# Kernel tuning notes

Measured on AMD Instinct MI355X. Metric: run time of the kernel, lower is better.

Reference implementation:

```python
import jax, jax.numpy as jnp
import numpy as np

N, D, HID, G, E2 = 2048, 256, 128, 8, 16384


def _mlp(h, w1, b1, g, be, w2, b2):
    # Linear -> ReLU -> BatchNorm1d (training mode, biased batch var) -> Linear
    h = jax.nn.relu(h @ w1 + b1)
    mu = h.mean(axis=0)
    var = ((h - mu) ** 2).mean(axis=0)
    h = (h - mu) / jnp.sqrt(var + 1e-5) * g + be
    return h @ w2 + b2


def setup_inputs() -> dict:
    key = jax.random.key(0)
    ks = jax.random.split(key, 12)
    x = jax.random.normal(ks[0], (N, D), jnp.float32)
    src = jax.random.randint(ks[1], (E2,), 0, N)
    dst = jax.random.randint(ks[2], (E2,), 0, N)
    src = jnp.where(src == dst, (src + 1) % N, src)  # no self loops
    edge_index = jnp.stack([jnp.concatenate([src, dst]),
                            jnp.concatenate([dst, src])])  # symmetric
    batch = jnp.sort(jax.random.randint(ks[3], (N,), 0, G))
    def lin(k, i, o):
        return 0.1 * jax.random.normal(k, (i, o), jnp.float32)
    out = dict(x=x, edge_index=edge_index, batch=batch)
    dims = [(1, HID, HID), (HID, HID, HID), (HID, HID, 1)]
    names = [("w11", "b11", "g1", "be1", "w12", "b12"),
             ("w21", "b21", "g2", "be2", "w22", "b22"),
             ("w31", "b31", "g3", "be3", "w32", "b32")]
    k = 4
    for (i, h, o), n in zip(dims, names):
        out[n[0]] = lin(ks[k], i, h)
        out[n[1]] = jnp.zeros((h,), jnp.float32)
        out[n[2]] = jnp.ones((h,), jnp.float32)
        out[n[3]] = jnp.zeros((h,), jnp.float32)
        out[n[4]] = lin(ks[k + 1], h, o)
        out[n[5]] = jnp.zeros((o,), jnp.float32)
        k += 2
    return out


def reference(x, edge_index, batch,
              w11, b11, g1, be1, w12, b12,
              w21, b21, g2, be2, w22, b22,
              w31, b31, g3, be3, w32, b32):
    n = x.shape[0]
    # dense adjacency from edge_index; L = D - A (unnormalized graph Laplacian)
    A = jnp.zeros((n, n), x.dtype).at[edge_index[0], edge_index[1]].set(1.0)
    deg = A.sum(axis=1)
    # entropy term: V = x*(Lx) - x*(Ax) + A(x*x), Lx = deg*x - Ax
    Ax = A @ x
    V = x * (deg[:, None] * x - Ax) - x * Ax + A @ (x * x)
    V = jnp.linalg.norm(V, axis=1)  # [n]
    # per-graph softmax over the batch segments
    mx = jax.ops.segment_max(V, batch, num_segments=G)
    ex = jnp.exp(V - mx[batch])
    P = ex / jax.ops.segment_sum(ex, batch, num_segments=G)[batch]
    P = jnp.where(P == 0.0, 1.0, P)
    ent = -P * jnp.log(P)  # [n]

    # GINConv (eps=0): mlp(x + sum_{j in N(i)} x_j) = mlp(x + A @ x)
    def gin(h, w1, b1, g, be, w2, b2):
        return _mlp(h + A @ h, w1, b1, g, be, w2, b2)

    h = gin(ent[:, None], w11, b11, g1, be1, w12, b12)
    h = gin(h, w21, b21, g2, be2, w22, b22)
    h = gin(h, w31, b31, g3, be3, w32, b32)
    p = jax.nn.sigmoid(h[:, 0])  # [n] node probabilities

    gamma = ent.sum()
    loss = gamma - jnp.vdot(ent, p) + jnp.vdot(p, A @ p)

    # greedy conditional expectation (sequential MIS-style selection)
    order = jnp.argsort(-p)

    def step(carry, idx):
        dummy, sel, rej = carry
        nb = A[idx] > 0.0  # neighbor mask [n]
        deg0 = ~jnp.any(nb)
        sel = sel.at[idx].set(sel[idx] | deg0)  # isolated node -> selected
        eligible = (~rej[idx]) & (~sel[idx])
        s = jnp.where(nb, 0.0, dummy).at[idx].set(1.0)
        li = gamma - jnp.vdot(ent, s) + jnp.vdot(s, A @ s)
        accept = eligible & (li <= loss)
        sel = sel.at[idx].set(sel[idx] | accept)
        rej = rej | (nb & accept)
        dummy = jnp.where(accept, s, dummy)
        return (dummy, sel, rej), None

    init = (p, jnp.zeros(n, dtype=bool), jnp.zeros(n, dtype=bool))
    (dummy, sel, rej), _ = jax.lax.scan(step, init, order)

    # graph reconstruction (masked instead of compacted, for static shapes)
    mask = sel.astype(x.dtype)
    x_pooled = x * mask[:, None]
    A2 = A @ A
    A3 = A2 @ A
    eye = jnp.eye(n, dtype=x.dtype)
    adj_pooled = (1.0 - eye) * jnp.clip(A2 + A3, 0.0, 1.0) * (mask[:, None] * mask[None, :])
    batch_pooled = jnp.where(sel, batch, -1)
    return x_pooled, adj_pooled, sel, batch_pooled, loss
```

## Files before the change

### kernel.cpp

```cpp
#include <hip/hip_runtime.h>
#include <math.h>

#define NN 2048
#define DIMF 256
#define HIDN 128
#define NG 8
#define NEDGES 32768
#define W32 32
#define TRI_CAP 131072
#define TRI_LDS 4864

typedef unsigned long long u64;
typedef unsigned char u8;
typedef unsigned short u16;

__global__ void k_init(u64* __restrict__ rowbits, int* __restrict__ segstart) {
  int i = blockIdx.x * blockDim.x + threadIdx.x;
  for (int k = i; k < NN * W32; k += gridDim.x * blockDim.x) rowbits[k] = 0ull;
  if (i <= NG) segstart[i] = NN;
}

__global__ void k_edges(const int* __restrict__ ei, u64* __restrict__ rowbits) {
  int e = blockIdx.x * blockDim.x + threadIdx.x;
  if (e >= NEDGES) return;
  int u = ei[e], v = ei[NEDGES + e];
  atomicOr(&rowbits[((size_t)u << 5) + (v >> 6)], 1ull << (v & 63));
}

__global__ void k_deg(const u64* __restrict__ rowbits, int* __restrict__ deg,
                      const int* __restrict__ batch, int* __restrict__ segstart) {
  int i = blockIdx.x * blockDim.x + threadIdx.x;
  if (i >= NN) return;
  int c = 0;
  for (int w = 0; w < W32; ++w) c += __popcll(rowbits[(i << 5) + w]);
  deg[i] = c;
  if (i == 0 || batch[i] != batch[i - 1]) segstart[batch[i]] = i;
}

__global__ void k_scan2048(const int* __restrict__ in, int* __restrict__ out) {
  __shared__ int part[256];
  int t = threadIdx.x;
  int v[8]; int s = 0;
  for (int k = 0; k < 8; ++k) { v[k] = in[t * 8 + k]; s += v[k]; }
  part[t] = s;
  __syncthreads();
  for (int off = 1; off < 256; off <<= 1) {
    int y = (t >= off) ? part[t - off] : 0;
    __syncthreads();
    part[t] += y;
    __syncthreads();
  }
  int run = part[t] - s;
  for (int k = 0; k < 8; ++k) { out[t * 8 + k] = run; run += v[k]; }
  if (t == 255) out[NN] = part[255];
}

__global__ void k_extract(const u64* __restrict__ rowbits, const int* __restrict__ rp,
                          int* __restrict__ col, int* __restrict__ cnt) {
  int i = blockIdx.x * blockDim.x + threadIdx.x;
  if (i >= NN) return;
  const u64* ri = rowbits + ((size_t)i << 5);
  int o = rp[i];
  for (int w = 0; w < W32; ++w) {
    u64 b = ri[w];
    while (b) { col[o++] = (w << 6) + __builtin_ctzll(b); b &= b - 1; }
  }
  int c = 0;
  for (int e = rp[i]; e < o; ++e) {
    const u64* ra = rowbits + ((size_t)col[e] << 5);
    for (int w = 0; w < W32; ++w) c += __popcll(ra[w] & ri[w]);
  }
  cnt[i] = c;
}

__global__ void k_trifill(const u64* __restrict__ rowbits, const int* __restrict__ rp,
                          const int* __restrict__ col, const int* __restrict__ tp,
                          int2* __restrict__ tri) {
  int i = blockIdx.x * blockDim.x + threadIdx.x;
  if (i >= NN) return;
  const u64* ri = rowbits + ((size_t)i << 5);
  int o = tp[i];
  for (int e = rp[i]; e < rp[i + 1]; ++e) {
    int a = col[e];
    const u64* ra = rowbits + ((size_t)a << 5);
    for (int w = 0; w < W32; ++w) {
      u64 b = ra[w] & ri[w];
      while (b) {
        int j = (w << 6) + __builtin_ctzll(b);
        if (o < TRI_CAP) tri[o] = make_int2(a, j);
        ++o;
        b &= b - 1;
      }
    }
  }
}

__global__ void k_V(const float* __restrict__ x, const int* __restrict__ rp,
                    const int* __restrict__ col, float* __restrict__ V) {
  int i = blockIdx.x; int t = threadIdx.x;
  float xi = x[i * DIMF + t];
  float s1 = 0.f, s2 = 0.f;
  int r0 = rp[i], r1 = rp[i + 1];
  for (int e = r0; e < r1; ++e) {
    float xj = x[col[e] * DIMF + t];
    s1 += xj; s2 += xj * xj;
  }
  float dg = (float)(r1 - r0);
  float val = dg * xi * xi - 2.f * xi * s1 + s2;
  __shared__ double red[DIMF];
  red[t] = (double)val * (double)val;
  __syncthreads();
  for (int off = DIMF / 2; off > 0; off >>= 1) { if (t < off) red[t] += red[t + off]; __syncthreads(); }
  if (t == 0) V[i] = (float)sqrt(red[0]);
}

__global__ void k_soft(const float* __restrict__ V, const int* __restrict__ segstart,
                       float* __restrict__ ent, double* __restrict__ seggamma) {
  int g = blockIdx.x; int t = threadIdx.x;
  int s = segstart[g];
  int e = NN;
  for (int gg = g + 1; gg <= NG; ++gg) { int v = segstart[gg]; if (v < e) e = v; }
  if (s >= e) { if (t == 0) seggamma[g] = 0.0; return; }
  __shared__ float fm[256];
  __shared__ double dd[256];
  float m = -3.0e38f;
  for (int i = s + t; i < e; i += 256) m = fmaxf(m, V[i]);
  fm[t] = m; __syncthreads();
  for (int off = 128; off > 0; off >>= 1) { if (t < off) fm[t] = fmaxf(fm[t], fm[t + off]); __syncthreads(); }
  float mx = fm[0];
  __syncthreads();
  double sum = 0.0;
  for (int i = s + t; i < e; i += 256) sum += exp((double)V[i] - (double)mx);
  dd[t] = sum; __syncthreads();
  for (int off = 128; off > 0; off >>= 1) { if (t < off) dd[t] += dd[t + off]; __syncthreads(); }
  double tot = dd[0];
  __syncthreads();
  double gs = 0.0;
  for (int i = s + t; i < e; i += 256) {
    double P = exp((double)V[i] - (double)mx) / tot;
    float ev = (P > 0.0) ? (float)(-P * log(P)) : 0.f;
    ent[i] = ev;
    gs += (double)ev;
  }
  dd[t] = gs; __syncthreads();
  for (int off = 128; off > 0; off >>= 1) { if (t < off) dd[t] += dd[t + off]; __syncthreads(); }
  if (t == 0) seggamma[g] = dd[0];
}

__global__ void k_agg1(const float* __restrict__ ent, const int* __restrict__ rp,
                       const int* __restrict__ col, float* __restrict__ agg) {
  int i = blockIdx.x * blockDim.x + threadIdx.x;
  if (i >= NN) return;
  float a = ent[i];
  for (int e = rp[i]; e < rp[i + 1]; ++e) a += ent[col[e]];
  agg[i] = a;
}

template<int FROMAGG>
__global__ void k_bn(const float* __restrict__ src, const float* __restrict__ w1,
                     const float* __restrict__ b1, const float* __restrict__ g,
                     const float* __restrict__ be, float* __restrict__ scale,
                     float* __restrict__ shift) {
  int k = blockIdx.x; int tid = threadIdx.x;
  __shared__ double red[256];
  float wk = 0.f, bk = 0.f;
  if (FROMAGG) { wk = w1[k]; bk = b1[k]; }
  double s = 0.0;
  for (int i = tid; i < NN; i += 256) {
    float v;
    if (FROMAGG) { v = src[i] * wk + bk; v = v > 0.f ? v : 0.f; }
    else v = src[i * HIDN + k];
    s += (double)v;
  }
  red[tid] = s; __syncthreads();
  for (int off = 128; off > 0; off >>= 1) { if (tid < off) red[tid] += red[tid + off]; __syncthreads(); }
  double mu = red[0] / NN;
  __syncthreads();
  double vv = 0.0;
  for (int i = tid; i < NN; i += 256) {
    float v;
    if (FROMAGG) { v = src[i] * wk + bk; v = v > 0.f ? v : 0.f; }
    else v = src[i * HIDN + k];
    double dv = (double)v - mu; vv += dv * dv;
  }
  red[tid] = vv; __syncthreads();
  for (int off = 128; off > 0; off >>= 1) { if (tid < off) red[tid] += red[tid + off]; __syncthreads(); }
  if (tid == 0) {
    float var = (float)(red[0] / NN);
    float sc = g[k] / sqrtf(var + 1e-5f);
    scale[k] = sc;
    shift[k] = be[k] - (float)mu * sc;
  }
}

template<int PRE, int RELU>
__global__ void k_mm(const float* __restrict__ in, const float* __restrict__ Wm,
                     const float* __restrict__ bias, const float* __restrict__ scale,
                     const float* __restrict__ shift, const float* __restrict__ lw,
                     const float* __restrict__ lb, float* __restrict__ out) {
  __shared__ float ti[8][HIDN];
  int r0 = blockIdx.x * 8; int t = threadIdx.x;
  for (int r = 0; r < 8; ++r) {
    float v;
    if (PRE == 2) {
      v = in[r0 + r] * lw[t] + lb[t];
      v = v > 0.f ? v : 0.f;
      v = v * scale[t] + shift[t];
    } else {
      v = in[(r0 + r) * HIDN + t];
      if (PRE == 1) v = v * scale[t] + shift[t];
    }
    ti[r][t] = v;
  }
  __syncthreads();
  float acc[8];
  #pragma unroll
  for (int r = 0; r < 8; ++r) acc[r] = 0.f;
  for (int k = 0; k < HIDN; ++k) {
    float w = Wm[k * HIDN + t];
    #pragma unroll
    for (int r = 0; r < 8; ++r) acc[r] += ti[r][k] * w;
  }
  for (int r = 0; r < 8; ++r) {
    float v = acc[r] + bias[t];
    if (RELU) v = fmaxf(v, 0.f);
    out[(r0 + r) * HIDN + t] = v;
  }
}

__global__ void k_agg128(const float* __restrict__ h, const int* __restrict__ rp,
                         const int* __restrict__ col, float* __restrict__ agg) {
  int i = blockIdx.x; int t = threadIdx.x;
  float a = h[i * HIDN + t];
  for (int e = rp[i]; e < rp[i + 1]; ++e) a += h[col[e] * HIDN + t];
  agg[i * HIDN + t] = a;
}

__global__ void k_lin3(const float* __restrict__ tn, const float* __restrict__ scale,
                       const float* __restrict__ shift, const float* __restrict__ w32,
                       const float* __restrict__ b32, float* __restrict__ p) {
  int i = blockIdx.x; int t = threadIdx.x;
  float v = (tn[i * HIDN + t] * scale[t] + shift[t]) * w32[t];
  __shared__ float red[HIDN];
  red[t] = v; __syncthreads();
  for (int off = 64; off > 0; off >>= 1) { if (t < off) red[t] += red[t + off]; __syncthreads(); }
  if (t == 0) {
    float h3 = red[0] + b32[0];
    p[i] = 1.f / (1.f + expf(-h3));
  }
}

__global__ void k_q0(const float* __restrict__ p, const float* __restrict__ ent,
                     const int* __restrict__ rp, const int* __restrict__ col,
                     float* __restrict__ q0, float* __restrict__ e0) {
  int i = blockIdx.x * blockDim.x + threadIdx.x;
  if (i >= NN) return;
  float s = 0.f, es = 0.f;
  for (int e = rp[i]; e < rp[i + 1]; ++e) {
    int j = col[e];
    float pj = p[j];
    s += pj; es += ent[j] * pj;
  }
  q0[i] = s; e0[i] = es;
}

__global__ void __launch_bounds__(1024, 1) k_sortloss(
    const float* __restrict__ p, const float* __restrict__ ent,
    const float* __restrict__ q0, const double* __restrict__ seggamma,
    double* __restrict__ scal, int* __restrict__ order) {
  __shared__ u64 s[NN];
  __shared__ double rr[32];
  int t = threadIdx.x;
  double a = 0.0, b = 0.0;
  for (int i = t; i < NN; i += 1024) {
    a += (double)ent[i] * (double)p[i];
    b += (double)p[i] * (double)q0[i];
  }
  for (int off = 32; off; off >>= 1) { a += __shfl_down(a, off); b += __shfl_down(b, off); }
  if ((t & 63) == 0) { rr[(t >> 6) * 2] = a; rr[(t >> 6) * 2 + 1] = b; }
  for (int k = t; k < NN; k += 1024) {
    unsigned bb = __float_as_uint(p[k]);
    unsigned ss = (bb & 0x80000000u) ? ~bb : (bb | 0x80000000u);
    s[k] = ((u64)(~ss) << 32) | (unsigned)k;
  }
  __syncthreads();
  if (t == 0) {
    double A = 0.0, Bb = 0.0, gamma = 0.0;
    for (int i = 0; i < 16; ++i) { A += rr[2 * i]; Bb += rr[2 * i + 1]; }
    for (int g = 0; g < NG; ++g) gamma += seggamma[g];
    scal[0] = gamma; scal[1] = A; scal[2] = Bb; scal[3] = gamma - A + Bb;
  }
  for (int k = 2; k <= NN; k <<= 1) {
    for (int j = k >> 1; j > 0; j >>= 1) {
      for (int i = t; i < NN; i += 1024) {
        int ixj = i ^ j;
        if (ixj > i) {
          bool up = ((i & k) == 0);
          u64 aa = s[i], bb = s[ixj];
          if ((aa > bb) == up) { s[i] = bb; s[ixj] = aa; }
        }
      }
      __syncthreads();
    }
  }
  order[t] = (int)(s[t] & 0xFFFFFFFFull);
  order[t + 1024] = (int)(s[t + 1024] & 0xFFFFFFFFull);
}

#define DPP2(ctrl)                                                                        \
  a += __int_as_float(__builtin_amdgcn_update_dpp(0, __float_as_int(a), ctrl, 0xf, 0xf, true)); \
  b += __int_as_float(__builtin_amdgcn_update_dpp(0, __float_as_int(b), ctrl, 0xf, 0xf, true));

__device__ __forceinline__ void red2(float& a, float& b) {
  DPP2(0x111)
  DPP2(0x112)
  DPP2(0x114)
  DPP2(0x118)
  DPP2(0x142)
  DPP2(0x143)
  a = __int_as_float(__builtin_amdgcn_readlane(__float_as_int(a), 63));
  b = __int_as_float(__builtin_amdgcn_readlane(__float_as_int(b), 63));
}

__global__ void __launch_bounds__(1024, 1) k_greedy(
    const int* __restrict__ rp, const int* __restrict__ col,
    const int* __restrict__ tp, const int2* __restrict__ tri,
    const int* __restrict__ order, const float* __restrict__ p,
    const float* __restrict__ ent, const float* __restrict__ q0,
    const float* __restrict__ e0, const double* __restrict__ scal,
    u8* __restrict__ selb_g) {
  __shared__ float2 dq[NN];
  __shared__ float2 ee[NN];
  __shared__ u16 colL[NEDGES];
  __shared__ u16 ordl[NN];
  __shared__ uint2 rtP[NN + 1];
  __shared__ ushort2 triL[TRI_LDS];
  __shared__ unsigned decidedL[64], selL[64];
  __shared__ unsigned maskL[2];
  __shared__ float4 svA[2][16];
  __shared__ float svQ[2][16];
  int t = threadIdx.x;
  int w = t >> 6, lane = t & 63;

  for (int i = t; i < NN; i += 1024) {
    dq[i] = make_float2(p[i], q0[i]);
    ee[i] = make_float2(ent[i], e0[i]);
    ordl[i] = (u16)order[i];
    int tv0 = tp[i]; if (tv0 > 65535) tv0 = 65535;
    int tv1 = tp[i + 1]; if (tv1 > 65535) tv1 = 65535;
    rtP[i] = make_uint2((unsigned)rp[i] | ((unsigned)tv0 << 16),
                        (unsigned)rp[i + 1] | ((unsigned)tv1 << 16));
  }
  for (int i = t; i < NEDGES; i += 1024) colL[i] = (u16)col[i];
  for (int i = t; i < TRI_LDS; i += 1024) {
    int2 ab = tri[i];
    triL[i] = make_ushort2((u16)(ab.x & 2047), (u16)(ab.y & 2047));
  }
  if (t < 64) { decidedL[t] = 0u; selL[t] = 0u; }
  if (t < 2) maskL[t] = 0u;
  double gamma = scal[0], loss = scal[3];
  double ed = scal[1], dAd = scal[2];
  __syncthreads();
  for (int i = t; i < NN; i += 1024) {
    if (((rtP[i].y & 0xffffu) - (rtP[i].x & 0xffffu)) == 0u) {
      atomicOr(&decidedL[i >> 5], 1u << (i & 31));
      atomicOr(&selL[i >> 5], 1u << (i & 31));
    }
  }
  __syncthreads();

  int pos = 0, rc = 0;
  while (pos < NN) {
    int b = rc & 1; ++rc;
    int step = pos + w;
    if (step < NN) {
      int idx = ordl[step];
      if (!((decidedL[idx >> 5] >> (idx & 31)) & 1u)) {
        uint2 rt = rtP[idx];
        int r0 = rt.x & 0xffff, r1 = rt.y & 0xffff;
        int t0 = rt.x >> 16, t1 = rt.y >> 16;
        float2 dqi = dq[idx];
        float2 eei = ee[idx];
        float s2 = 0.f, st = 0.f;
        for (int e = r0 + lane; e < r1; e += 64) {
          float2 v = dq[colL[e]];
          s2 -= v.y * v.x;
        }
        if (t1 <= TRI_LDS) {
          for (int e = t0 + lane; e < t1; e += 64) {
            ushort2 ab = triL[e];
            st += dq[ab.x].x * dq[ab.y].x;
          }
        } else {
          int g0 = tp[idx], g1 = tp[idx + 1];
          if (g0 > TRI_CAP) g0 = TRI_CAP;
          if (g1 > TRI_CAP) g1 = TRI_CAP;
          for (int e = g0 + lane; e < g1; e += 64) {
            int2 ab = tri[e];
            st += dq[ab.x].x * dq[ab.y].x;
          }
        }
        red2(s2, st);
        float d0 = 1.f - dqi.x;
        float S1 = -eei.y + eei.x * d0;
        float S2 = s2 + dqi.y * d0;
        float sn = -dqi.y;
        double cross = 2.0 * (double)d0 * (double)sn + (double)st;
        double li = gamma - (ed + (double)S1) + (dAd + 2.0 * (double)S2 + cross);
        if (li <= loss && lane == 0) {
          svA[b][w] = make_float4(S1, S2, d0, st);
          svQ[b][w] = dqi.y;
          atomicOr(&maskL[b], 1u << w);
        }
      }
    }
    __syncthreads();
    unsigned mask = maskL[b];
    if (mask == 0u) { pos += 16; continue; }
    int k = __builtin_ctz(mask);
    int idx = ordl[pos + k];
    float4 A = svA[b][k];
    float qi = svQ[b][k];
    uint2 rt = rtP[idx];
    int r0 = rt.x & 0xffff, r1 = rt.y & 0xffff;
    {
      double cross = 2.0 * (double)A.z * (double)(-qi) + (double)A.w;
      ed += (double)A.x;
      dAd += 2.0 * (double)A.y + cross;
    }
    for (int e = r0 + w; e < r1; e += 16) {
      int a = colL[e];
      float da = -dq[a].x;
      if (da != 0.f) {
        float ea = ee[a].x;
        uint2 art = rtP[a];
        int b0 = art.x & 0xffff, b1 = art.y & 0xffff;
        for (int eb = b0 + lane; eb < b1; eb += 64) {
          int bb = colL[eb];
          atomicAdd(&dq[bb].y, da);
          atomicAdd(&ee[bb].y, ea * da);
        }
      }
    }
    {
      float ei = ee[idx].x;
      for (int e = r0 + t; e < r1; e += 1024) {
        int bb = colL[e];
        atomicAdd(&dq[bb].y, A.z);
        atomicAdd(&ee[bb].y, ei * A.z);
      }
    }
    __syncthreads();
    if (t == 0) {
      dq[idx].x = 1.f;
      atomicOr(&decidedL[idx >> 5], 1u << (idx & 31));
      atomicOr(&selL[idx >> 5], 1u << (idx & 31));
      maskL[b] = 0u;
    }
    for (int e = r0 + t; e < r1; e += 1024) {
      int j = colL[e];
      dq[j].x = 0.f;
      atomicOr(&decidedL[j >> 5], 1u << (j & 31));
    }
    __syncthreads();
    pos = pos + k + 1;
  }
  for (int i = t; i < NN; i += 1024)
    selb_g[i] = (u8)((selL[i >> 5] >> (i & 31)) & 1u);
}

__global__ void k_reach(const u64* __restrict__ src, const int* __restrict__ rp,
                        const int* __restrict__ col, u64* __restrict__ dst) {
  int node = blockIdx.x * 2 + (threadIdx.x >> 5);
  int w = threadIdx.x & 31;
  u64 acc = 0;
  for (int e = rp[node]; e < rp[node + 1]; ++e) acc |= src[((size_t)col[e] << 5) + w];
  dst[((size_t)node << 5) + w] = acc;
}

__global__ void k_out(const u64* __restrict__ row2, const u64* __restrict__ row3,
                      const u8* __restrict__ selb, const float* __restrict__ x,
                      const int* __restrict__ batch, const double* __restrict__ scal,
                      float* __restrict__ o_x, float* __restrict__ o_adj,
                      float* __restrict__ o_sel, float* __restrict__ o_bat,
                      float* __restrict__ o_loss) {
  int idx = blockIdx.x * blockDim.x + threadIdx.x;
  {
    int i = idx >> 11, j = idx & 2047;
    int wo = (i << 5) + (j >> 6);
    u64 b = (row2[wo] | row3[wo]) >> (j & 63);
    o_adj[idx] = ((b & 1ull) && i != j && selb[i] && selb[j]) ? 1.f : 0.f;
  }
  if (idx < NN * DIMF) {
    int i = idx >> 8;
    o_x[idx] = selb[i] ? x[idx] : 0.f;
  }
  if (idx < NN) {
    o_sel[idx] = selb[idx] ? 1.f : 0.f;
    o_bat[idx] = selb[idx] ? (float)batch[idx] : -1.f;
  }
  if (idx == 0) o_loss[0] = (float)scal[3];
}

extern "C" void kernel_launch(void* const* d_in, const int* in_sizes, int n_in,
                              void* d_out, int out_size, void* d_ws, size_t ws_size,
                              hipStream_t stream) {
  const float* x    = (const float*)d_in[0];
  const int*   ei   = (const int*)d_in[1];
  const int*   batch= (const int*)d_in[2];
  const float* w11  = (const float*)d_in[3];
  const float* b11  = (const float*)d_in[4];
  const float* g1   = (const float*)d_in[5];
  const float* be1  = (const float*)d_in[6];
  const float* w12  = (const float*)d_in[7];
  const float* b12  = (const float*)d_in[8];
  const float* w21  = (const float*)d_in[9];
  const float* b21  = (const float*)d_in[10];
  const float* g2   = (const float*)d_in[11];
  const float* be2  = (const float*)d_in[12];
  const float* w22  = (const float*)d_in[13];
  const float* b22  = (const float*)d_in[14];
  const float* w31  = (const float*)d_in[15];
  const float* b31  = (const float*)d_in[16];
  const float* g3   = (const float*)d_in[17];
  const float* be3  = (const float*)d_in[18];
  const float* w32  = (const float*)d_in[19];
  const float* b32  = (const float*)d_in[20];

  char* wsb = (char*)d_ws;
  size_t cur = 0;
  auto alloc = [&](size_t bytes) -> void* {
    void* pp = wsb + cur;
    cur += (bytes + 255) & ~(size_t)255;
    return pp;
  };
  u64*    rowbits = (u64*)alloc((size_t)NN * W32 * 8);
  u64*    row2    = (u64*)alloc((size_t)NN * W32 * 8);
  u64*    row3    = (u64*)alloc((size_t)NN * W32 * 8);
  double* seggam  = (double*)alloc(NG * 8);
  double* scal    = (double*)alloc(4 * 8);
  int*    deg     = (int*)alloc(NN * 4);
  int*    rowptr  = (int*)alloc((NN + 1) * 4);
  int*    colx    = (int*)alloc(65536 * 4);
  int*    tricnt  = (int*)alloc(NN * 4);
  int*    triptr  = (int*)alloc((NN + 1) * 4);
  int2*   tri     = (int2*)alloc((size_t)TRI_CAP * 8);
  int*    segst   = (int*)alloc((NG + 1) * 4);
  int*    order   = (int*)alloc(NN * 4);
  float*  ent     = (float*)alloc(NN * 4);
  float*  V       = (float*)alloc(NN * 4);
  float*  p       = (float*)alloc(NN * 4);
  float*  q0      = (float*)alloc(NN * 4);
  float*  e0      = (float*)alloc(NN * 4);
  float*  agg1    = (float*)alloc(NN * 4);
  float*  scale   = (float*)alloc(HIDN * 4);
  float*  shift   = (float*)alloc(HIDN * 4);
  float*  tA      = (float*)alloc((size_t)NN * HIDN * 4);
  float*  tB      = (float*)alloc((size_t)NN * HIDN * 4);
  float*  tC      = (float*)alloc((size_t)NN * HIDN * 4);
  u8*     selb    = (u8*)alloc(NN);

  float* out    = (float*)d_out;
  float* o_x    = out;
  float* o_adj  = out + 524288;
  float* o_sel  = out + 4718592;
  float* o_bat  = out + 4720640;
  float* o_loss = out + 4722688;

  k_init<<<64, 256, 0, stream>>>(rowbits, segst);
  k_edges<<<128, 256, 0, stream>>>(ei, rowbits);
  k_deg<<<8, 256, 0, stream>>>(rowbits, deg, batch, segst);
  k_scan2048<<<1, 256, 0, stream>>>(deg, rowptr);
  k_extract<<<8, 256, 0, stream>>>(rowbits, rowptr, colx, tricnt);
  k_scan2048<<<1, 256, 0, stream>>>(tricnt, triptr);
  k_trifill<<<8, 256, 0, stream>>>(rowbits, rowptr, colx, triptr, tri);
  k_V<<<NN, 256, 0, stream>>>(x, rowptr, colx, V);
  k_soft<<<NG, 256, 0, stream>>>(V, segst, ent, seggam);

  k_agg1<<<8, 256, 0, stream>>>(ent, rowptr, colx, agg1);
  k_bn<1><<<HIDN, 256, 0, stream>>>(agg1, w11, b11, g1, be1, scale, shift);
  k_mm<2, 0><<<NN / 8, HIDN, 0, stream>>>(agg1, w12, b12, scale, shift, w11, b11, tB);
  k_agg128<<<NN, HIDN, 0, stream>>>(tB, rowptr, colx, tC);
  k_mm<0, 1><<<NN / 8, HIDN, 0, stream>>>(tC, w21, b21, scale, shift, (const float*)0, (const float*)0, tA);
  k_bn<0><<<HIDN, 256, 0, stream>>>(tA, (const float*)0, (const float*)0, g2, be2, scale, shift);
  k_mm<1, 0><<<NN / 8, HIDN, 0, stream>>>(tA, w22, b22, scale, shift, (const float*)0, (const float*)0, tB);
  k_agg128<<<NN, HIDN, 0, stream>>>(tB, rowptr, colx, tC);
  k_mm<0, 1><<<NN / 8, HIDN, 0, stream>>>(tC, w31, b31, scale, shift, (const float*)0, (const float*)0, tA);
  k_bn<0><<<HIDN, 256, 0, stream>>>(tA, (const float*)0, (const float*)0, g3, be3, scale, shift);
  k_lin3<<<NN, HIDN, 0, stream>>>(tA, scale, shift, w32, b32, p);

  k_q0<<<8, 256, 0, stream>>>(p, ent, rowptr, colx, q0, e0);
  k_sortloss<<<1, 1024, 0, stream>>>(p, ent, q0, seggam, scal, order);
  k_greedy<<<1, 1024, 0, stream>>>(rowptr, colx, triptr, tri, order, p, ent, q0, e0, scal, selb);

  k_reach<<<NN / 2, 64, 0, stream>>>(rowbits, rowptr, colx, row2);
  k_reach<<<NN / 2, 64, 0, stream>>>(row2, rowptr, colx, row3);
  k_out<<<NN * NN / 256, 256, 0, stream>>>(row2, row3, selb, x, batch, scal,
                                           o_x, o_adj, o_sel, o_bat, o_loss);

  (void)in_sizes; (void)n_in; (void)out_size; (void)ws_size;
}
```

Before: 1.091 ms.

## Compact undecided candidates in greedy loop and fold q0/loss/degree-scan kernels

```diff
diff --git a/kernel.cpp b/kernel.cpp
--- a/kernel.cpp
+++ b/kernel.cpp
@@ -27,14 +27,29 @@
   atomicOr(&rowbits[((size_t)u << 5) + (v >> 6)], 1ull << (v & 63));
 }
 
-__global__ void k_deg(const u64* __restrict__ rowbits, int* __restrict__ deg,
-                      const int* __restrict__ batch, int* __restrict__ segstart) {
-  int i = blockIdx.x * blockDim.x + threadIdx.x;
-  if (i >= NN) return;
-  int c = 0;
-  for (int w = 0; w < W32; ++w) c += __popcll(rowbits[(i << 5) + w]);
-  deg[i] = c;
-  if (i == 0 || batch[i] != batch[i - 1]) segstart[batch[i]] = i;
+__global__ void k_degscan(const u64* __restrict__ rowbits, const int* __restrict__ batch,
+                          int* __restrict__ segstart, int* __restrict__ out) {
+  __shared__ int part[256];
+  int t = threadIdx.x;
+  int v[8]; int s = 0;
+  for (int k = 0; k < 8; ++k) {
+    int node = t * 8 + k;
+    int c = 0;
+    for (int w = 0; w < W32; ++w) c += __popcll(rowbits[((size_t)node << 5) + w]);
+    v[k] = c; s += c;
+    if (node == 0 || batch[node] != batch[node - 1]) segstart[batch[node]] = node;
+  }
+  part[t] = s;
+  __syncthreads();
+  for (int off = 1; off < 256; off <<= 1) {
+    int y = (t >= off) ? part[t - off] : 0;
+    __syncthreads();
+    part[t] += y;
+    __syncthreads();
+  }
+  int run = part[t] - s;
+  for (int k = 0; k < 8; ++k) { out[t * 8 + k] = run; run += v[k]; }
+  if (t == 255) out[NN] = part[255];
 }
 
 __global__ void k_scan2048(const int* __restrict__ in, int* __restrict__ out) {
@@ -250,54 +265,24 @@
   }
 }
 
-__global__ void k_q0(const float* __restrict__ p, const float* __restrict__ ent,
-                     const int* __restrict__ rp, const int* __restrict__ col,
-                     float* __restrict__ q0, float* __restrict__ e0) {
-  int i = blockIdx.x * blockDim.x + threadIdx.x;
-  if (i >= NN) return;
-  float s = 0.f, es = 0.f;
-  for (int e = rp[i]; e < rp[i + 1]; ++e) {
-    int j = col[e];
-    float pj = p[j];
-    s += pj; es += ent[j] * pj;
-  }
-  q0[i] = s; e0[i] = es;
-}
-
-__global__ void __launch_bounds__(1024, 1) k_sortloss(
-    const float* __restrict__ p, const float* __restrict__ ent,
-    const float* __restrict__ q0, const double* __restrict__ seggamma,
-    double* __restrict__ scal, int* __restrict__ order) {
+__global__ void __launch_bounds__(1024, 1) k_sort(const float* __restrict__ p,
+                                                  int* __restrict__ order) {
   __shared__ u64 s[NN];
-  __shared__ double rr[32];
   int t = threadIdx.x;
-  double a = 0.0, b = 0.0;
-  for (int i = t; i < NN; i += 1024) {
-    a += (double)ent[i] * (double)p[i];
-    b += (double)p[i] * (double)q0[i];
-  }
-  for (int off = 32; off; off >>= 1) { a += __shfl_down(a, off); b += __shfl_down(b, off); }
-  if ((t & 63) == 0) { rr[(t >> 6) * 2] = a; rr[(t >> 6) * 2 + 1] = b; }
   for (int k = t; k < NN; k += 1024) {
-    unsigned bb = __float_as_uint(p[k]);
-    unsigned ss = (bb & 0x80000000u) ? ~bb : (bb | 0x80000000u);
+    unsigned b = __float_as_uint(p[k]);
+    unsigned ss = (b & 0x80000000u) ? ~b : (b | 0x80000000u);
     s[k] = ((u64)(~ss) << 32) | (unsigned)k;
   }
   __syncthreads();
-  if (t == 0) {
-    double A = 0.0, Bb = 0.0, gamma = 0.0;
-    for (int i = 0; i < 16; ++i) { A += rr[2 * i]; Bb += rr[2 * i + 1]; }
-    for (int g = 0; g < NG; ++g) gamma += seggamma[g];
-    scal[0] = gamma; scal[1] = A; scal[2] = Bb; scal[3] = gamma - A + Bb;
-  }
   for (int k = 2; k <= NN; k <<= 1) {
     for (int j = k >> 1; j > 0; j >>= 1) {
       for (int i = t; i < NN; i += 1024) {
         int ixj = i ^ j;
         if (ixj > i) {
           bool up = ((i & k) == 0);
-          u64 aa = s[i], bb = s[ixj];
-          if ((aa > bb) == up) { s[i] = bb; s[ixj] = aa; }
+          u64 a = s[i], b = s[ixj];
+          if ((a > b) == up) { s[i] = b; s[ixj] = a; }
         }
       }
       __syncthreads();
@@ -326,9 +311,8 @@
     const int* __restrict__ rp, const int* __restrict__ col,
     const int* __restrict__ tp, const int2* __restrict__ tri,
     const int* __restrict__ order, const float* __restrict__ p,
-    const float* __restrict__ ent, const float* __restrict__ q0,
-    const float* __restrict__ e0, const double* __restrict__ scal,
-    u8* __restrict__ selb_g) {
+    const float* __restrict__ ent, const double* __restrict__ seggam,
+    double* __restrict__ scal, u8* __restrict__ selb_g) {
   __shared__ float2 dq[NN];
   __shared__ float2 ee[NN];
   __shared__ u16 colL[NEDGES];
@@ -339,12 +323,15 @@
   __shared__ unsigned maskL[2];
   __shared__ float4 svA[2][16];
   __shared__ float svQ[2][16];
+  __shared__ int   svP[2][16];
+  __shared__ u64 wbalL[16];
+  __shared__ double rr[36];
   int t = threadIdx.x;
   int w = t >> 6, lane = t & 63;
 
   for (int i = t; i < NN; i += 1024) {
-    dq[i] = make_float2(p[i], q0[i]);
-    ee[i] = make_float2(ent[i], e0[i]);
+    dq[i].x = p[i];
+    ee[i].x = ent[i];
     ordl[i] = (u16)order[i];
     int tv0 = tp[i]; if (tv0 > 65535) tv0 = 65535;
     int tv1 = tp[i + 1]; if (tv1 > 65535) tv1 = 65535;
@@ -358,69 +345,129 @@
   }
   if (t < 64) { decidedL[t] = 0u; selL[t] = 0u; }
   if (t < 2) maskL[t] = 0u;
-  double gamma = scal[0], loss = scal[3];
-  double ed = scal[1], dAd = scal[2];
   __syncthreads();
   for (int i = t; i < NN; i += 1024) {
-    if (((rtP[i].y & 0xffffu) - (rtP[i].x & 0xffffu)) == 0u) {
+    int r0 = rtP[i].x & 0xffff, r1 = rtP[i].y & 0xffff;
+    float qs = 0.f, es = 0.f;
+    for (int e = r0; e < r1; ++e) {
+      int j = colL[e];
+      float pj = dq[j].x;
+      qs += pj; es += ee[j].x * pj;
+    }
+    dq[i].y = qs; ee[i].y = es;
+    if (r0 == r1) {
       atomicOr(&decidedL[i >> 5], 1u << (i & 31));
       atomicOr(&selL[i >> 5], 1u << (i & 31));
     }
   }
   __syncthreads();
+  {
+    double a = 0.0, b = 0.0;
+    for (int i = t; i < NN; i += 1024) {
+      a += (double)ee[i].x * (double)dq[i].x;
+      b += (double)dq[i].x * (double)dq[i].y;
+    }
+    for (int off = 32; off; off >>= 1) { a += __shfl_down(a, off); b += __shfl_down(b, off); }
+    if ((t & 63) == 0) { rr[(t >> 6) * 2] = a; rr[(t >> 6) * 2 + 1] = b; }
+  }
+  __syncthreads();
+  if (t == 0) {
+    double A = 0.0, Bb = 0.0, g = 0.0;
+    for (int i = 0; i < 16; ++i) { A += rr[2 * i]; Bb += rr[2 * i + 1]; }
+    for (int gg = 0; gg < NG; ++gg) g += seggam[gg];
+    rr[32] = g; rr[33] = A; rr[34] = Bb; rr[35] = g - A + Bb;
+    scal[0] = g; scal[1] = A; scal[2] = Bb; scal[3] = g - A + Bb;
+  }
+  __syncthreads();
+  double gamma = rr[32], loss = rr[35];
+  double ed = rr[33], dAd = rr[34];
+  __syncthreads();
 
   int pos = 0, rc = 0;
   while (pos < NN) {
-    int b = rc & 1; ++rc;
-    int step = pos + w;
-    if (step < NN) {
-      int idx = ordl[step];
-      if (!((decidedL[idx >> 5] >> (idx & 31)) & 1u)) {
-        uint2 rt = rtP[idx];
-        int r0 = rt.x & 0xffff, r1 = rt.y & 0xffff;
-        int t0 = rt.x >> 16, t1 = rt.y >> 16;
-        float2 dqi = dq[idx];
-        float2 eei = ee[idx];
-        float s2 = 0.f, st = 0.f;
-        for (int e = r0 + lane; e < r1; e += 64) {
-          float2 v = dq[colL[e]];
-          s2 -= v.y * v.x;
+    int b2 = rc & 1; ++rc;
+    {
+      int P = pos + t;
+      int f = 0;
+      if (P < NN) {
+        int ix = ordl[P];
+        f = !((decidedL[ix >> 5] >> (ix & 31)) & 1u);
+      }
+      u64 bal = __ballot(f);
+      if (lane == 0) wbalL[w] = bal;
+    }
+    __syncthreads();
+    int myc = __popcll(wbalL[lane & 15]);
+    int pre = myc;
+    #pragma unroll
+    for (int d = 1; d < 16; d <<= 1) {
+      int v = __shfl_up(pre, d, 16);
+      if ((lane & 15) >= d) pre += v;
+    }
+    int total = __shfl(pre, 15, 16);
+    int exc = pre - myc;
+    int myP = -1;
+    if (w < total) {
+      bool hit = (exc <= w) && (w < pre);
+      u64 bal2 = __ballot(hit) & 0xffffull;
+      int word = (int)__builtin_ctzll(bal2);
+      int excw = __shfl(exc, word, 16);
+      int r = w - excw;
+      u64 bits = wbalL[word];
+      for (int k2 = 0; k2 < r; ++k2) bits &= bits - 1;
+      myP = pos + (word << 6) + (int)__builtin_ctzll(bits);
+    }
+    if (myP >= 0) {
+      if (lane == 0) svP[b2][w] = myP;
+      int idx = ordl[myP];
+      uint2 rt = rtP[idx];
+      int r0 = rt.x & 0xffff, r1 = rt.y & 0xffff;
+      int t0 = rt.x >> 16, t1 = rt.y >> 16;
+      float2 dqi = dq[idx];
+      float2 eei = ee[idx];
+      float s2 = 0.f, st = 0.f;
+      for (int e = r0 + lane; e < r1; e += 64) {
+        float2 v = dq[colL[e]];
+        s2 -= v.y * v.x;
+      }
+      if (t1 <= TRI_LDS) {
+        for (int e = t0 + lane; e < t1; e += 64) {
+          ushort2 ab = triL[e];
+          st += dq[ab.x].x * dq[ab.y].x;
         }
-        if (t1 <= TRI_LDS) {
-          for (int e = t0 + lane; e < t1; e += 64) {
-            ushort2 ab = triL[e];
-            st += dq[ab.x].x * dq[ab.y].x;
-          }
-        } else {
-          int g0 = tp[idx], g1 = tp[idx + 1];
-          if (g0 > TRI_CAP) g0 = TRI_CAP;
-          if (g1 > TRI_CAP) g1 = TRI_CAP;
-          for (int e = g0 + lane; e < g1; e += 64) {
-            int2 ab = tri[e];
-            st += dq[ab.x].x * dq[ab.y].x;
-          }
+      } else {
+        int g0 = tp[idx], g1 = tp[idx + 1];
+        if (g0 > TRI_CAP) g0 = TRI_CAP;
+        if (g1 > TRI_CAP) g1 = TRI_CAP;
+        for (int e = g0 + lane; e < g1; e += 64) {
+          int2 ab = tri[e];
+          st += dq[ab.x].x * dq[ab.y].x;
         }
-        red2(s2, st);
-        float d0 = 1.f - dqi.x;
-        float S1 = -eei.y + eei.x * d0;
-        float S2 = s2 + dqi.y * d0;
-        float sn = -dqi.y;
-        double cross = 2.0 * (double)d0 * (double)sn + (double)st;
-        double li = gamma - (ed + (double)S1) + (dAd + 2.0 * (double)S2 + cross);
-        if (li <= loss && lane == 0) {
-          svA[b][w] = make_float4(S1, S2, d0, st);
-          svQ[b][w] = dqi.y;
-          atomicOr(&maskL[b], 1u << w);
-        }
-      }
-    }
-    __syncthreads();
-    unsigned mask = maskL[b];
-    if (mask == 0u) { pos += 16; continue; }
+      }
+      red2(s2, st);
+      float d0 = 1.f - dqi.x;
+      float S1 = -eei.y + eei.x * d0;
+      float S2 = s2 + dqi.y * d0;
+      float sn = -dqi.y;
+      double cross = 2.0 * (double)d0 * (double)sn + (double)st;
+      double li = gamma - (ed + (double)S1) + (dAd + 2.0 * (double)S2 + cross);
+      if (li <= loss && lane == 0) {
+        svA[b2][w] = make_float4(S1, S2, d0, st);
+        svQ[b2][w] = dqi.y;
+        atomicOr(&maskL[b2], 1u << w);
+      }
+    }
+    __syncthreads();
+    unsigned mask = maskL[b2];
+    if (mask == 0u) {
+      pos = (total >= 16) ? (svP[b2][15] + 1) : (pos + 1024);
+      continue;
+    }
     int k = __builtin_ctz(mask);
-    int idx = ordl[pos + k];
-    float4 A = svA[b][k];
-    float qi = svQ[b][k];
+    int Pk = svP[b2][k];
+    int idx = ordl[Pk];
+    float4 A = svA[b2][k];
+    float qi = svQ[b2][k];
     uint2 rt = rtP[idx];
     int r0 = rt.x & 0xffff, r1 = rt.y & 0xffff;
     {
@@ -455,7 +502,7 @@
       dq[idx].x = 1.f;
       atomicOr(&decidedL[idx >> 5], 1u << (idx & 31));
       atomicOr(&selL[idx >> 5], 1u << (idx & 31));
-      maskL[b] = 0u;
+      maskL[b2] = 0u;
     }
     for (int e = r0 + t; e < r1; e += 1024) {
       int j = colL[e];
@@ -463,7 +510,7 @@
       atomicOr(&decidedL[j >> 5], 1u << (j & 31));
     }
     __syncthreads();
-    pos = pos + k + 1;
+    pos = Pk + 1;
   }
   for (int i = t; i < NN; i += 1024)
     selb_g[i] = (u8)((selL[i >> 5] >> (i & 31)) & 1u);
@@ -539,7 +586,6 @@
   u64*    row3    = (u64*)alloc((size_t)NN * W32 * 8);
   double* seggam  = (double*)alloc(NG * 8);
   double* scal    = (double*)alloc(4 * 8);
-  int*    deg     = (int*)alloc(NN * 4);
   int*    rowptr  = (int*)alloc((NN + 1) * 4);
   int*    colx    = (int*)alloc(65536 * 4);
   int*    tricnt  = (int*)alloc(NN * 4);
@@ -550,8 +596,6 @@
   float*  ent     = (float*)alloc(NN * 4);
   float*  V       = (float*)alloc(NN * 4);
   float*  p       = (float*)alloc(NN * 4);
-  float*  q0      = (float*)alloc(NN * 4);
-  float*  e0      = (float*)alloc(NN * 4);
   float*  agg1    = (float*)alloc(NN * 4);
   float*  scale   = (float*)alloc(HIDN * 4);
   float*  shift   = (float*)alloc(HIDN * 4);
@@ -569,8 +613,7 @@
 
   k_init<<<64, 256, 0, stream>>>(rowbits, segst);
   k_edges<<<128, 256, 0, stream>>>(ei, rowbits);
-  k_deg<<<8, 256, 0, stream>>>(rowbits, deg, batch, segst);
-  k_scan2048<<<1, 256, 0, stream>>>(deg, rowptr);
+  k_degscan<<<1, 256, 0, stream>>>(rowbits, batch, segst, rowptr);
   k_extract<<<8, 256, 0, stream>>>(rowbits, rowptr, colx, tricnt);
   k_scan2048<<<1, 256, 0, stream>>>(tricnt, triptr);
   k_trifill<<<8, 256, 0, stream>>>(rowbits, rowptr, colx, triptr, tri);
@@ -589,9 +632,8 @@
   k_bn<0><<<HIDN, 256, 0, stream>>>(tA, (const float*)0, (const float*)0, g3, be3, scale, shift);
   k_lin3<<<NN, HIDN, 0, stream>>>(tA, scale, shift, w32, b32, p);
 
-  k_q0<<<8, 256, 0, stream>>>(p, ent, rowptr, colx, q0, e0);
-  k_sortloss<<<1, 1024, 0, stream>>>(p, ent, q0, seggam, scal, order);
-  k_greedy<<<1, 1024, 0, stream>>>(rowptr, colx, triptr, tri, order, p, ent, q0, e0, scal, selb);
+  k_sort<<<1, 1024, 0, stream>>>(p, order);
+  k_greedy<<<1, 1024, 0, stream>>>(rowptr, colx, triptr, tri, order, p, ent, seggam, scal, selb);
 
   k_reach<<<NN / 2, 64, 0, stream>>>(rowbits, rowptr, colx, row2);
   k_reach<<<NN / 2, 64, 0, stream>>>(row2, rowptr, colx, row3);
```

After: 1.479 ms. 1.36x slower.
